# Kernel tuning notes

Measured on AMD Instinct MI355X. Metric: run time of the kernel, lower is better.

## Reference

```python
import jax, jax.numpy as jnp
import numpy as np

N = 50000
E = 640000
F_IN = 96
H1 = 128
H2 = 128
NUM_CLASSES = 256
NGRAM = 3
D1 = 32
L2_EPS = 1e-12


def _prop(xt, src, dst, ew):
    # weighted scatter-add aggregation: out[dst] += ew * xt[src]
    return jax.ops.segment_sum(ew[:, None] * xt[src], dst, num_segments=N)


def _digcn_layer(x, W_mi, W_mo, W_sk, b_mi, b_mo, b_si, b_so, C_in, C_out,
                 ei_in, ew_in, ei_out, ew_out):
    x_sk = x @ W_sk  # skip transform shared by in/out branches
    ic = (_prop(x @ W_mi, ei_in[0], ei_in[1], ew_in) + b_mi
          + _prop(x_sk, ei_in[0], ei_in[1], ew_in) + b_si)
    oc = (_prop(x @ W_mo, ei_out[0], ei_out[1], ew_out) + b_mo
          + _prop(x_sk, ei_out[0], ei_out[1], ew_out) + b_so)
    return C_in * ic + C_out * oc  # C_* are [N,1] vector coefficients


def setup_inputs() -> dict:
    key = jax.random.key(0)
    ks = jax.random.split(key, 32)
    s = 0.05
    d = {
        'x': jax.random.normal(ks[0], (N, F_IN), dtype=jnp.float32),
        'edge_index_in': jax.random.randint(ks[1], (2, E), 0, N, dtype=jnp.int32),
        'edge_weight_in': jax.random.uniform(ks[2], (E,), dtype=jnp.float32),
        'edge_index_out': jax.random.randint(ks[3], (2, E), 0, N, dtype=jnp.int32),
        'edge_weight_out': jax.random.uniform(ks[4], (E,), dtype=jnp.float32),
        'pe_table': jax.random.normal(ks[5], (NGRAM, D1), dtype=jnp.float32) * s,
    }
    dims = [(F_IN, H1), (H1, H1), (H1, H2)]
    ki = 6
    for li, (di, do) in enumerate(dims, start=1):
        d[f'W{li}_main_in'] = jax.random.normal(ks[ki], (di, do), dtype=jnp.float32) * s; ki += 1
        d[f'W{li}_main_out'] = jax.random.normal(ks[ki], (di, do), dtype=jnp.float32) * s; ki += 1
        d[f'W{li}_skip'] = jax.random.normal(ks[ki], (di, do), dtype=jnp.float32) * s; ki += 1
        d[f'b{li}_main_in'] = jax.random.normal(ks[ki], (do,), dtype=jnp.float32) * s; ki += 1
        d[f'b{li}_main_out'] = jax.random.normal(ks[ki], (do,), dtype=jnp.float32) * s; ki += 1
        d[f'b{li}_skip_in'] = jax.random.normal(ks[ki], (do,), dtype=jnp.float32) * s; ki += 1
        d[f'b{li}_skip_out'] = jax.random.normal(ks[ki], (do,), dtype=jnp.float32) * s; ki += 1
        d[f'C{li}_in'] = 1.0 + jax.random.normal(ks[ki], (N, 1), dtype=jnp.float32) * 0.02; ki += 1
        d[f'C{li}_out'] = 1.0 + jax.random.normal(ks[ki], (N, 1), dtype=jnp.float32) * 0.02; ki += 1
    k2 = jax.random.split(ks[ki], 4)
    d['res1_W'] = jax.random.normal(k2[0], (F_IN, H1), dtype=jnp.float32) * s
    d['res1_b'] = jax.random.normal(k2[1], (H1,), dtype=jnp.float32) * s
    d['dec_W'] = jax.random.normal(k2[2], (H2, NUM_CLASSES), dtype=jnp.float32) * s
    d['dec_b'] = jax.random.normal(k2[3], (NUM_CLASSES,), dtype=jnp.float32) * s
    return d


def reference(x, edge_index_in, edge_weight_in, edge_index_out, edge_weight_out, pe_table,
              W1_main_in, W1_main_out, W1_skip, b1_main_in, b1_main_out, b1_skip_in, b1_skip_out, C1_in, C1_out,
              W2_main_in, W2_main_out, W2_skip, b2_main_in, b2_main_out, b2_skip_in, b2_skip_out, C2_in, C2_out,
              W3_main_in, W3_main_out, W3_skip, b3_main_in, b3_main_out, b3_skip_in, b3_skip_out, C3_in, C3_out,
              res1_W, res1_b, dec_W, dec_b):
    # learnable positional encoding: x viewed as [N, ngram, d1] + pe[pos]
    x = (x.reshape(-1, NGRAM, D1) + pe_table[None]).reshape(-1, NGRAM * D1)

    h1 = _digcn_layer(x, W1_main_in, W1_main_out, W1_skip, b1_main_in, b1_main_out,
                      b1_skip_in, b1_skip_out, C1_in, C1_out,
                      edge_index_in, edge_weight_in, edge_index_out, edge_weight_out)
    h1 = jax.nn.relu(h1 + (x @ res1_W + res1_b))  # residual_proj_1 (96 -> 128)

    h2 = _digcn_layer(h1, W2_main_in, W2_main_out, W2_skip, b2_main_in, b2_main_out,
                      b2_skip_in, b2_skip_out, C2_in, C2_out,
                      edge_index_in, edge_weight_in, edge_index_out, edge_weight_out)
    h2 = jax.nn.relu(h2 + h1)  # identity residual (128 == 128)

    h3 = _digcn_layer(h2, W3_main_in, W3_main_out, W3_skip, b3_main_in, b3_main_out,
                      b3_skip_in, b3_skip_out, C3_in, C3_out,
                      edge_index_in, edge_weight_in, edge_index_out, edge_weight_out)
    h3 = h3 + h2  # residual_proj_3 is Identity (hidden1 == hidden2)

    norm = jnp.maximum(jnp.linalg.norm(h3, axis=1, keepdims=True), L2_EPS)
    emb = h3 / norm  # F.normalize, eps=1e-12
    logits = emb @ dec_W + dec_b
    return jax.nn.log_softmax(logits, axis=-1), emb
```

## Files before the change

kernel.cpp:

```cpp
#include <hip/hip_runtime.h>
#include <hip/hip_bf16.h>

typedef unsigned short ushort_t;
typedef __attribute__((ext_vector_type(8))) short bf16x8;
typedef __attribute__((ext_vector_type(4))) float f32x4;

__device__ __forceinline__ float bf2f(ushort_t u) {
    union { unsigned int i; float f; } v; v.i = ((unsigned int)u) << 16; return v.f;
}
__device__ __forceinline__ ushort_t f2bf(float f) {
    unsigned int u = __float_as_uint(f);
    unsigned int r = u + 0x7FFFu + ((u >> 16) & 1u);
    return (ushort_t)(r >> 16);
}
__device__ __forceinline__ float ldf(const void* p, size_t i, int isf) {
    return isf ? ((const float*)p)[i] : bf2f(((const ushort_t*)p)[i]);
}

__global__ void init_k(int* __restrict__ cntI, int* __restrict__ cntO, int n2,
                       const void* __restrict__ x, int* __restrict__ flag) {
    int i = blockIdx.x * 256 + threadIdx.x;
    if (i < n2) { cntI[i] = 0; cntO[i] = 0; }
    if (blockIdx.x == 0) {
        int t = threadIdx.x;
        const float* xf = (const float*)x;
        int bad = 0;
        for (int k = t; k < 2048; k += 256) {
            unsigned int u = __float_as_uint(xf[k]);
            unsigned int e = (u >> 23) & 0xFFu;
            if (e >= 0xC0u) bad = 1;
        }
        __shared__ int s_bad;
        if (t == 0) s_bad = 0;
        __syncthreads();
        if (bad) atomicOr(&s_bad, 1);
        __syncthreads();
        if (t == 0) flag[0] = s_bad ? 0 : 1;
    }
}

__global__ void count_both_k(const int* __restrict__ eiI, const int* __restrict__ eiO,
                             int* __restrict__ cntI, int* __restrict__ cntO,
                             int E, int egrid) {
    int set = blockIdx.x >= egrid ? 1 : 0;
    int e = (blockIdx.x - set * egrid) * 256 + threadIdx.x;
    if (e >= E) return;
    const int* ei = set ? eiO : eiI;
    int* cnt = set ? cntO : cntI;
    atomicAdd(&cnt[ei[E + e]], 1);
}

__global__ __launch_bounds__(256) void scan1_k(const int* __restrict__ cntA, const int* __restrict__ cntB,
                                               int* __restrict__ offA, int* __restrict__ offB,
                                               int* __restrict__ sums, int n, int nChunks) {
    int set = blockIdx.y;
    const int* cnt = set ? cntB : cntA;
    int* off = set ? offB : offA;
    __shared__ int s[256];
    int t = threadIdx.x;
    int idx = blockIdx.x * 1024 + t * 4;
    int v[4];
#pragma unroll
    for (int i = 0; i < 4; ++i) v[i] = (idx + i < n) ? cnt[idx + i] : 0;
    int tsum = v[0] + v[1] + v[2] + v[3];
    s[t] = tsum;
    __syncthreads();
    for (int d = 1; d < 256; d <<= 1) {
        int x = (t >= d) ? s[t - d] : 0;
        __syncthreads();
        s[t] += x;
        __syncthreads();
    }
    int run = s[t] - tsum;
    if (t == 255) sums[set * nChunks + blockIdx.x] = s[255];
#pragma unroll
    for (int i = 0; i < 4; ++i) { if (idx + i < n) off[idx + i] = run; run += v[i]; }
}

__global__ __launch_bounds__(256) void scan2_k(int* __restrict__ sums, int nChunks) {
    __shared__ int s[256];
    int t = threadIdx.x;
    for (int set = 0; set < 2; ++set) {
        int v = (t < nChunks) ? sums[set * nChunks + t] : 0;
        s[t] = v;
        __syncthreads();
        for (int d = 1; d < 256; d <<= 1) {
            int x = (t >= d) ? s[t - d] : 0;
            __syncthreads();
            s[t] += x;
            __syncthreads();
        }
        if (t < nChunks) sums[set * nChunks + t] = s[t] - v;
        __syncthreads();
    }
}

__global__ __launch_bounds__(256) void scan3_k(int* __restrict__ offA, int* __restrict__ offB,
                                               const int* __restrict__ sums, int n, int nChunks, int E) {
    int set = blockIdx.y;
    int* off = set ? offB : offA;
    int base = sums[set * nChunks + blockIdx.x];
    int idx = blockIdx.x * 1024 + threadIdx.x * 4;
#pragma unroll
    for (int i = 0; i < 4; ++i) { if (idx + i < n) off[idx + i] += base; }
    if (blockIdx.x == 0 && threadIdx.x == 0) off[n] = E;
}

__global__ void fill_both_k(const int* __restrict__ eiI, const void* __restrict__ ewI,
                            const int* __restrict__ eiO, const void* __restrict__ ewO,
                            const int* __restrict__ offI, const int* __restrict__ offO,
                            int* __restrict__ curI, int* __restrict__ curO,
                            uint2* __restrict__ prI, uint2* __restrict__ prO,
                            int E, int egrid, const int* __restrict__ flagp) {
    int isf = *flagp;
    int set = blockIdx.x >= egrid ? 1 : 0;
    int e = (blockIdx.x - set * egrid) * 256 + threadIdx.x;
    if (e >= E) return;
    const int* ei = set ? eiO : eiI;
    const void* ew = set ? ewO : ewI;
    const int* off = set ? offO : offI;
    int* cur = set ? curO : curI;
    uint2* pr = set ? prO : prI;
    int d = ei[E + e];
    int p = off[d] + atomicAdd(&cur[d], 1);
    pr[p] = make_uint2((unsigned)ei[e], __float_as_uint(ldf(ew, e, isf)));
}

struct PrepJob { const void* A; const void* B; ushort_t* dst; int K; int colOff; int cshift; int n; int blkBase; };
struct PrepJobsT { PrepJob j[8]; };
__global__ __launch_bounds__(256) void prep_all_k(PrepJobsT jobs, const int* __restrict__ flagp) {
    int isf = *flagp;
    int b = blockIdx.x;
    int ji = 0;
#pragma unroll
    for (int t = 1; t < 8; ++t) if (b >= jobs.j[t].blkBase) ji = t;
    PrepJob jb = jobs.j[ji];
    int i = (b - jb.blkBase) * 256 + threadIdx.x;
    if (i >= jb.n) return;
    int cmask = (1 << jb.cshift) - 1;
    int k = i >> jb.cshift, c = i & cmask;
    int Cw = cmask + 1;
    float v = ldf(jb.A, (size_t)k * Cw + c, isf);
    if (jb.B) v += ldf(jb.B, (size_t)k * Cw + c, isf);
    jb.dst[(size_t)(jb.colOff + c) * jb.K + k] = f2bf(v);
}

struct BiasJob { const void* a; const void* b; float* dst; int n; };
struct BiasJobs { BiasJob j[8]; };
__global__ void prep_bias_k(BiasJobs jobs, const int* __restrict__ flagp) {
    int isf = *flagp;
    BiasJob jb = jobs.j[blockIdx.x];
    int t = threadIdx.x;
    if (t < jb.n) {
        float v = ldf(jb.a, t, isf);
        if (jb.b) v += ldf(jb.b, t, isf);
        jb.dst[t] = v;
    }
}

template<int K, int DOUT>
__global__ __launch_bounds__(256) void gemm_mfma_k(
    const ushort_t* __restrict__ A, const ushort_t* __restrict__ Wt,
    ushort_t* __restrict__ Y, int M) {
    constexpr int NT = DOUT / 16;
    int tid = threadIdx.x;
    int wave = tid >> 6, lane = tid & 63;
    int q = lane >> 4, l15 = lane & 15;
    int arow = blockIdx.x * 64 + wave * 16 + l15;
    int rowc = arow < M ? arow : M - 1;
    f32x4 acc[NT];
#pragma unroll
    for (int t = 0; t < NT; ++t) acc[t] = (f32x4){0.f, 0.f, 0.f, 0.f};
#pragma unroll
    for (int kc = 0; kc < K; kc += 32) {
        bf16x8 a = *(const bf16x8*)(A + (size_t)rowc * K + kc + q * 8);
#pragma unroll
        for (int t = 0; t < NT; ++t) {
            bf16x8 b = *(const bf16x8*)(Wt + (size_t)(t * 16 + l15) * K + kc + q * 8);
            acc[t] = __builtin_amdgcn_mfma_f32_16x16x32_bf16(a, b, acc[t], 0, 0, 0);
        }
    }
    int outRowBase = blockIdx.x * 64 + wave * 16 + q * 4;
#pragma unroll
    for (int t = 0; t < NT; ++t) {
        int col = t * 16 + l15;
#pragma unroll
        for (int i = 0; i < 4; ++i) {
            int r = outRowBase + i;
            if (r < M) Y[(size_t)r * DOUT + col] = f2bf(acc[t][i]);
        }
    }
}

__global__ __launch_bounds__(256) void gemm_mfma_x_k(
    const void* __restrict__ X, const ushort_t* __restrict__ Wt,
    ushort_t* __restrict__ Y, int M, const void* __restrict__ pe,
    const int* __restrict__ flagp) {
    constexpr int K = 96, DOUT = 384, NT = DOUT / 16;
    __shared__ float pes[96];
    int isf = *flagp;
    int tid = threadIdx.x;
    if (tid < 96) pes[tid] = ldf(pe, tid, isf);
    __syncthreads();
    int wave = tid >> 6, lane = tid & 63;
    int q = lane >> 4, l15 = lane & 15;
    int arow = blockIdx.x * 64 + wave * 16 + l15;
    int rowc = arow < M ? arow : M - 1;
    f32x4 acc[NT];
#pragma unroll
    for (int t = 0; t < NT; ++t) acc[t] = (f32x4){0.f, 0.f, 0.f, 0.f};
#pragma unroll
    for (int kc = 0; kc < K; kc += 32) {
        float va[8];
        size_t base = (size_t)rowc * K + kc + q * 8;
        if (isf) {
            float4 u0 = *(const float4*)((const float*)X + base);
            float4 u1 = *(const float4*)((const float*)X + base + 4);
            va[0] = u0.x; va[1] = u0.y; va[2] = u0.z; va[3] = u0.w;
            va[4] = u1.x; va[5] = u1.y; va[6] = u1.z; va[7] = u1.w;
        } else {
            const ushort_t* xp = (const ushort_t*)X + base;
#pragma unroll
            for (int i = 0; i < 8; ++i) va[i] = bf2f(xp[i]);
        }
        bf16x8 a;
        short* ap = (short*)&a;
#pragma unroll
        for (int i = 0; i < 8; ++i) ap[i] = (short)f2bf(va[i] + pes[kc + q * 8 + i]);
#pragma unroll
        for (int t = 0; t < NT; ++t) {
            bf16x8 b = *(const bf16x8*)(Wt + (size_t)(t * 16 + l15) * K + kc + q * 8);
            acc[t] = __builtin_amdgcn_mfma_f32_16x16x32_bf16(a, b, acc[t], 0, 0, 0);
        }
    }
    int outRowBase = blockIdx.x * 64 + wave * 16 + q * 4;
#pragma unroll
    for (int t = 0; t < NT; ++t) {
        int col = t * 16 + l15;
#pragma unroll
        for (int i = 0; i < 4; ++i) {
            int r = outRowBase + i;
            if (r < M) Y[(size_t)r * DOUT + col] = f2bf(acc[t][i]);
        }
    }
}

__device__ __forceinline__ void accum8(float* acc, uint4 v, float w) {
    unsigned u[4] = {v.x, v.y, v.z, v.w};
#pragma unroll
    for (int i = 0; i < 4; ++i) {
        acc[2 * i]     = fmaf(w, __uint_as_float(u[i] << 16), acc[2 * i]);
        acc[2 * i + 1] = fmaf(w, __uint_as_float(u[i] & 0xFFFF0000u), acc[2 * i + 1]);
    }
}

__global__ __launch_bounds__(256) void prop_combine_k(
    const ushort_t* __restrict__ Y, int ldY,
    const int* __restrict__ offI, const uint2* __restrict__ prI,
    const int* __restrict__ offO, const uint2* __restrict__ prO,
    const void* __restrict__ Cin, const void* __restrict__ Cout,
    const float* __restrict__ bin, const float* __restrict__ bout,
    const ushort_t* __restrict__ res, int ldR, int colR, const float* __restrict__ res_b,
    ushort_t* __restrict__ H, int M, int relu, const int* __restrict__ flagp) {
    int isf = *flagp;
    int node = blockIdx.x * 4 + (threadIdx.x >> 6);
    int lane = threadIdx.x & 63;
    if (node >= M) return;
    int half = lane >> 5;
    int subq = (lane >> 4) & 1;
    int li   = lane & 15;
    int eI0 = offI[node], eI1 = offI[node + 1];
    int eO0 = offO[node], eO1 = offO[node + 1];
    int e0 = half ? eO0 : eI0;
    int e1 = half ? eO1 : eI1;
    const uint2* pairs = half ? prO : prI;
    const ushort_t* rowbase = Y + half * 128 + li * 8;
    int lenMax = max(eI1 - eI0, eO1 - eO0);
    float acc[8];
#pragma unroll
    for (int k = 0; k < 8; ++k) acc[k] = 0.f;
    for (int it = 0; it < lenMax; it += 4) {
        int eeA = e0 + it + subq;
        int eeB = eeA + 2;
        bool mA = eeA < e1, mB = eeB < e1;
        uint2 pa, pb;
        uint4 va, vb;
        if (mA) { pa = pairs[eeA]; va = *(const uint4*)(rowbase + (size_t)pa.x * ldY); }
        if (mB) { pb = pairs[eeB]; vb = *(const uint4*)(rowbase + (size_t)pb.x * ldY); }
        if (mA) accum8(acc, va, __uint_as_float(pa.y));
        if (mB) accum8(acc, vb, __uint_as_float(pb.y));
    }
    float other[8];
#pragma unroll
    for (int k = 0; k < 8; ++k) {
        acc[k] += __shfl_xor(acc[k], 16, 64);
        other[k] = __shfl_xor(acc[k], 32, 64);
    }
    int j = li * 8;
    float ci = ldf(Cin, node, isf), co = ldf(Cout, node, isf);
    uint4 rv = *(const uint4*)(res + (size_t)node * ldR + colR + j);
    float4 b0 = *(const float4*)(bin + j);
    float4 b1 = *(const float4*)(bin + j + 4);
    float4 c0 = *(const float4*)(bout + j);
    float4 c1 = *(const float4*)(bout + j + 4);
    float binv[8]  = {b0.x, b0.y, b0.z, b0.w, b1.x, b1.y, b1.z, b1.w};
    float boutv[8] = {c0.x, c0.y, c0.z, c0.w, c1.x, c1.y, c1.z, c1.w};
    float rbv[8] = {0.f, 0.f, 0.f, 0.f, 0.f, 0.f, 0.f, 0.f};
    if (res_b) {
        float4 r0 = *(const float4*)(res_b + j);
        float4 r1 = *(const float4*)(res_b + j + 4);
        rbv[0] = r0.x; rbv[1] = r0.y; rbv[2] = r0.z; rbv[3] = r0.w;
        rbv[4] = r1.x; rbv[5] = r1.y; rbv[6] = r1.z; rbv[7] = r1.w;
    }
    unsigned rw[4] = {rv.x, rv.y, rv.z, rv.w};
    float vo[8];
#pragma unroll
    for (int k = 0; k < 8; ++k) {
        float aiv = half ? other[k] : acc[k];
        float aov = half ? acc[k] : other[k];
        float r = (k & 1) ? __uint_as_float(rw[k >> 1] & 0xFFFF0000u)
                          : __uint_as_float(rw[k >> 1] << 16);
        float v = ci * (aiv + binv[k]) + co * (aov + boutv[k]) + r + rbv[k];
        if (relu) v = fmaxf(v, 0.f);
        vo[k] = v;
    }
    if ((lane >> 4) == 0) {
        uint4 outv;
        unsigned* op = (unsigned*)&outv;
#pragma unroll
        for (int k = 0; k < 4; ++k)
            op[k] = ((unsigned)f2bf(vo[2 * k + 1]) << 16) | (unsigned)f2bf(vo[2 * k]);
        *(uint4*)(H + (size_t)node * 128 + j) = outv;
    }
}

__global__ __launch_bounds__(256) void decoder_mfma_k(
    const ushort_t* __restrict__ h3, const ushort_t* __restrict__ Wdt,
    const float* __restrict__ biasDec, void* __restrict__ d_out, int M,
    const int* __restrict__ flagp) {
    __shared__ ushort_t embLds[64 * 136];
    __shared__ float sb[256];
    int isf = *flagp;
    int tid = threadIdx.x;
    sb[tid] = biasDec[tid];
    int rowBase = blockIdx.x * 64;
    {
        int r = tid >> 2;
        int c0 = (tid & 3) * 32;
        int grow = rowBase + r;
        uint4 u[4] = {};
        if (grow < M) {
            const uint4* p = (const uint4*)(h3 + (size_t)grow * 128 + c0);
            u[0] = p[0]; u[1] = p[1]; u[2] = p[2]; u[3] = p[3];
        }
        float v[32];
#pragma unroll
        for (int b = 0; b < 4; ++b) {
            unsigned w[4] = {u[b].x, u[b].y, u[b].z, u[b].w};
#pragma unroll
            for (int i = 0; i < 4; ++i) {
                v[b * 8 + 2 * i]     = bf2f((ushort_t)(w[i] & 0xffffu));
                v[b * 8 + 2 * i + 1] = bf2f((ushort_t)(w[i] >> 16));
            }
        }
        float ss = 0.f;
#pragma unroll
        for (int i = 0; i < 32; ++i) ss += v[i] * v[i];
        ss += __shfl_xor(ss, 1, 64);
        ss += __shfl_xor(ss, 2, 64);
        float inv = 1.0f / fmaxf(sqrtf(ss), 1e-12f);
#pragma unroll
        for (int i = 0; i < 32; ++i) v[i] *= inv;
        unsigned* lp = (unsigned*)&embLds[r * 136 + c0];
#pragma unroll
        for (int i = 0; i < 16; ++i)
            lp[i] = ((unsigned)f2bf(v[2 * i + 1]) << 16) | (unsigned)f2bf(v[2 * i]);
        if (grow < M) {
            if (isf) {
                float* op = (float*)d_out + (size_t)M * 256 + (size_t)grow * 128 + c0;
#pragma unroll
                for (int i = 0; i < 32; ++i) op[i] = v[i];
            } else {
                unsigned* op = (unsigned*)((ushort_t*)d_out + (size_t)M * 256 + (size_t)grow * 128 + c0);
#pragma unroll
                for (int i = 0; i < 16; ++i)
                    op[i] = ((unsigned)f2bf(v[2 * i + 1]) << 16) | (unsigned)f2bf(v[2 * i]);
            }
        }
    }
    __syncthreads();
    int wave = tid >> 6, lane = tid & 63, q = lane >> 4, l15 = lane & 15;
    f32x4 acc[16];
#pragma unroll
    for (int t = 0; t < 16; ++t) acc[t] = (f32x4){0.f, 0.f, 0.f, 0.f};
    int ldsRow = wave * 16 + l15;
#pragma unroll
    for (int kc = 0; kc < 128; kc += 32) {
        bf16x8 a = *(const bf16x8*)(&embLds[ldsRow * 136 + kc + q * 8]);
#pragma unroll
        for (int t = 0; t < 16; ++t) {
            bf16x8 b = *(const bf16x8*)(Wdt + (size_t)(t * 16 + l15) * 128 + kc + q * 8);
            acc[t] = __builtin_amdgcn_mfma_f32_16x16x32_bf16(a, b, acc[t], 0, 0, 0);
        }
    }
#pragma unroll
    for (int t = 0; t < 16; ++t) {
        float b = sb[t * 16 + l15];
        acc[t][0] += b; acc[t][1] += b; acc[t][2] += b; acc[t][3] += b;
    }
#pragma unroll
    for (int i = 0; i < 4; ++i) {
        int grow = rowBase + wave * 16 + q * 4 + i;
        float mx = acc[0][i];
#pragma unroll
        for (int t = 1; t < 16; ++t) mx = fmaxf(mx, acc[t][i]);
        mx = fmaxf(mx, __shfl_xor(mx, 1, 64));
        mx = fmaxf(mx, __shfl_xor(mx, 2, 64));
        mx = fmaxf(mx, __shfl_xor(mx, 4, 64));
        mx = fmaxf(mx, __shfl_xor(mx, 8, 64));
        float sm = 0.f;
#pragma unroll
        for (int t = 0; t < 16; ++t) sm += __expf(acc[t][i] - mx);
        sm += __shfl_xor(sm, 1, 64);
        sm += __shfl_xor(sm, 2, 64);
        sm += __shfl_xor(sm, 4, 64);
        sm += __shfl_xor(sm, 8, 64);
        float offv = mx + __logf(sm);
        if (grow < M) {
            if (isf) {
                float* op = (float*)d_out + (size_t)grow * 256 + l15;
#pragma unroll
                for (int t = 0; t < 16; ++t) op[t * 16] = acc[t][i] - offv;
            } else {
                ushort_t* op = (ushort_t*)d_out + (size_t)grow * 256 + l15;
#pragma unroll
                for (int t = 0; t < 16; ++t) op[t * 16] = f2bf(acc[t][i] - offv);
            }
        }
    }
}

extern "C" void kernel_launch(void* const* d_in, const int* in_sizes, int n_in,
                              void* d_out, int out_size, void* d_ws, size_t ws_size,
                              hipStream_t stream) {
    const int N = in_sizes[0] / 96;
    const int E = in_sizes[2];

    const void* x      = d_in[0];
    const int*  ei_in  = (const int*)d_in[1];
    const void* ew_in  = d_in[2];
    const int*  ei_out = (const int*)d_in[3];
    const void* ew_out = d_in[4];
    const void* pe     = d_in[5];

    const void *W_mi[3], *W_mo[3], *W_sk[3], *b_mi[3], *b_mo[3], *b_si[3], *b_so[3], *C_i[3], *C_o[3];
    for (int l = 0; l < 3; ++l) {
        int base = 6 + l * 9;
        W_mi[l] = d_in[base + 0];
        W_mo[l] = d_in[base + 1];
        W_sk[l] = d_in[base + 2];
        b_mi[l] = d_in[base + 3];
        b_mo[l] = d_in[base + 4];
        b_si[l] = d_in[base + 5];
        b_so[l] = d_in[base + 6];
        C_i[l]  = d_in[base + 7];
        C_o[l]  = d_in[base + 8];
    }
    const void* res1_W = d_in[33];
    const void* res1_b = d_in[34];
    const void* dec_W  = d_in[35];
    const void* dec_b  = d_in[36];

    char* ws = (char*)d_ws;
    size_t off = 0;
    auto alloc = [&](size_t bytes) -> void* {
        void* p = ws + off;
        off = (off + bytes + 255) & ~(size_t)255;
        return p;
    };
    const int nChunks = (N + 1023) / 1024;
    int*   flag    = (int*)alloc(4);
    int*   off_in  = (int*)alloc((size_t)(N + 1) * 4);
    int*   cnt_in  = (int*)alloc((size_t)2 * N * 4);
    int*   cur_in  = cnt_in + N;
    uint2* pr_in   = (uint2*)alloc((size_t)E * 8);
    int*   off_out = (int*)alloc((size_t)(N + 1) * 4);
    int*   cnt_out = (int*)alloc((size_t)2 * N * 4);
    int*   cur_out = cnt_out + N;
    uint2* pr_out  = (uint2*)alloc((size_t)E * 8);
    int*   sums    = (int*)alloc((size_t)2 * nChunks * 4);
    ushort_t* Wt1  = (ushort_t*)alloc((size_t)384 * 96 * 2);
    ushort_t* Wt2  = (ushort_t*)alloc((size_t)256 * 128 * 2);
    ushort_t* Wt3  = (ushort_t*)alloc((size_t)256 * 128 * 2);
    ushort_t* Wdt  = (ushort_t*)alloc((size_t)256 * 128 * 2);
    float* biasBlk = (float*)alloc((size_t)1152 * 4);
    float* bin1 = biasBlk, *bout1 = biasBlk + 128, *bin2 = biasBlk + 256, *bout2 = biasBlk + 384;
    float* bin3 = biasBlk + 512, *bout3 = biasBlk + 640, *res1b = biasBlk + 768, *decb = biasBlk + 896;
    ushort_t* Yb  = (ushort_t*)alloc((size_t)N * 384 * 2);
    ushort_t* H1  = (ushort_t*)alloc((size_t)N * 128 * 2);
    ushort_t* H2  = (ushort_t*)alloc((size_t)N * 128 * 2);
    ushort_t* H3  = H1;

    {
        int n2 = 2 * N;
        int g = (n2 + 255) / 256;
        init_k<<<g, 256, 0, stream>>>(cnt_in, cnt_out, n2, x, flag);
    }

    int egrid = (E + 255) / 256;
    count_both_k<<<2 * egrid, 256, 0, stream>>>(ei_in, ei_out, cnt_in, cnt_out, E, egrid);
    {
        dim3 g(nChunks, 2);
        scan1_k<<<g, 256, 0, stream>>>(cnt_in, cnt_out, off_in, off_out, sums, N, nChunks);
        scan2_k<<<1, 256, 0, stream>>>(sums, nChunks);
        scan3_k<<<g, 256, 0, stream>>>(off_in, off_out, sums, N, nChunks, E);
    }
    fill_both_k<<<2 * egrid, 256, 0, stream>>>(ei_in, ew_in, ei_out, ew_out,
        off_in, off_out, cur_in, cur_out, pr_in, pr_out, E, egrid, flag);

    {
        PrepJobsT pj;
        pj.j[0] = {W_mi[0], W_sk[0], Wt1, 96, 0,   7, 128 * 96, 0};
        pj.j[1] = {W_mo[0], W_sk[0], Wt1, 96, 128, 7, 128 * 96, 48};
        pj.j[2] = {res1_W, nullptr,  Wt1, 96, 256, 7, 128 * 96, 96};
        pj.j[3] = {W_mi[1], W_sk[1], Wt2, 128, 0,   7, 128 * 128, 144};
        pj.j[4] = {W_mo[1], W_sk[1], Wt2, 128, 128, 7, 128 * 128, 208};
        pj.j[5] = {W_mi[2], W_sk[2], Wt3, 128, 0,   7, 128 * 128, 272};
        pj.j[6] = {W_mo[2], W_sk[2], Wt3, 128, 128, 7, 128 * 128, 336};
        pj.j[7] = {dec_W, nullptr, Wdt, 128, 0, 8, 32768, 400};
        prep_all_k<<<528, 256, 0, stream>>>(pj, flag);
    }
    {
        BiasJobs jb;
        jb.j[0] = {b_mi[0], b_si[0], bin1, 128};
        jb.j[1] = {b_mo[0], b_so[0], bout1, 128};
        jb.j[2] = {b_mi[1], b_si[1], bin2, 128};
        jb.j[3] = {b_mo[1], b_so[1], bout2, 128};
        jb.j[4] = {b_mi[2], b_si[2], bin3, 128};
        jb.j[5] = {b_mo[2], b_so[2], bout3, 128};
        jb.j[6] = {res1_b, nullptr, res1b, 128};
        jb.j[7] = {dec_b, nullptr, decb, 256};
        prep_bias_k<<<8, 256, 0, stream>>>(jb, flag);
    }

    int gBlocks = (N + 63) / 64;
    int pgrid = (N + 3) / 4;

    gemm_mfma_x_k<<<gBlocks, 256, 0, stream>>>(x, Wt1, Yb, N, pe, flag);
    prop_combine_k<<<pgrid, 256, 0, stream>>>(Yb, 384,
        off_in, pr_in, off_out, pr_out,
        C_i[0], C_o[0], bin1, bout1, Yb, 384, 256, res1b, H1, N, 1, flag);
    gemm_mfma_k<128, 256><<<gBlocks, 256, 0, stream>>>(H1, Wt2, Yb, N);
    prop_combine_k<<<pgrid, 256, 0, stream>>>(Yb, 256,
        off_in, pr_in, off_out, pr_out,
        C_i[1], C_o[1], bin2, bout2, H1, 128, 0, (const float*)nullptr, H2, N, 1, flag);
    gemm_mfma_k<128, 256><<<gBlocks, 256, 0, stream>>>(H2, Wt3, Yb, N);
    prop_combine_k<<<pgrid, 256, 0, stream>>>(Yb, 256,
        off_in, pr_in, off_out, pr_out,
        C_i[2], C_o[2], bin3, bout3, H2, 128, 0, (const float*)nullptr, H3, N, 0, flag);
    decoder_mfma_k<<<gBlocks, 256, 0, stream>>>(H3, Wdt, decb, d_out, N, flag);
}
```

Baseline: 643.2 us.

## Build CSR via two-level bucketed binning with shared-memory histograms

Replaces per-node global atomic counting, the three-pass scan, and per-edge atomic scatter fill with a two-level counting sort. Edges are first binned into 64-node buckets using shared-memory histograms and one global atomic per bucket per block. A per-bucket kernel then sorts entries by local node in shared memory and writes the node offsets. This aims to cut global atomic contention and scattered writes during CSR construction. In exchange it adds a temporary buffer (aliased onto Yb), packs the local node id into the high bits of src (assumes src < 2^26), and relies on NB ≤ 1024 for the single-block scan.

```diff
diff --git a/kernel.cpp b/kernel.cpp
--- a/kernel.cpp
+++ b/kernel.cpp
@@ -17,10 +17,11 @@
     return isf ? ((const float*)p)[i] : bf2f(((const ushort_t*)p)[i]);
 }
 
-__global__ void init_k(int* __restrict__ cntI, int* __restrict__ cntO, int n2,
+__global__ void init_k(int* __restrict__ bcntI, int* __restrict__ bcntO,
+                       int* __restrict__ bcurI, int* __restrict__ bcurO, int NB,
                        const void* __restrict__ x, int* __restrict__ flag) {
     int i = blockIdx.x * 256 + threadIdx.x;
-    if (i < n2) { cntI[i] = 0; cntO[i] = 0; }
+    if (i < NB) { bcntI[i] = 0; bcntO[i] = 0; bcurI[i] = 0; bcurO[i] = 0; }
     if (blockIdx.x == 0) {
         int t = threadIdx.x;
         const float* xf = (const float*)x;
@@ -39,50 +40,44 @@
     }
 }
 
-__global__ void count_both_k(const int* __restrict__ eiI, const int* __restrict__ eiO,
-                             int* __restrict__ cntI, int* __restrict__ cntO,
-                             int E, int egrid) {
-    int set = blockIdx.x >= egrid ? 1 : 0;
-    int e = (blockIdx.x - set * egrid) * 256 + threadIdx.x;
-    if (e >= E) return;
+
+__global__ __launch_bounds__(256) void csr_count_k(
+    const int* __restrict__ eiI, const int* __restrict__ eiO,
+    int* __restrict__ bcntI, int* __restrict__ bcntO, int E, int nblk) {
+    int set = blockIdx.x >= nblk ? 1 : 0;
+    int blk = blockIdx.x - set * nblk;
     const int* ei = set ? eiO : eiI;
-    int* cnt = set ? cntO : cntI;
-    atomicAdd(&cnt[ei[E + e]], 1);
-}
-
-__global__ __launch_bounds__(256) void scan1_k(const int* __restrict__ cntA, const int* __restrict__ cntB,
-                                               int* __restrict__ offA, int* __restrict__ offB,
-                                               int* __restrict__ sums, int n, int nChunks) {
-    int set = blockIdx.y;
-    const int* cnt = set ? cntB : cntA;
-    int* off = set ? offB : offA;
-    __shared__ int s[256];
+    int* bcnt = set ? bcntO : bcntI;
+    __shared__ unsigned hist[1024];
     int t = threadIdx.x;
-    int idx = blockIdx.x * 1024 + t * 4;
-    int v[4];
-#pragma unroll
-    for (int i = 0; i < 4; ++i) v[i] = (idx + i < n) ? cnt[idx + i] : 0;
-    int tsum = v[0] + v[1] + v[2] + v[3];
-    s[t] = tsum;
-    __syncthreads();
-    for (int d = 1; d < 256; d <<= 1) {
-        int x = (t >= d) ? s[t - d] : 0;
-        __syncthreads();
-        s[t] += x;
-        __syncthreads();
-    }
-    int run = s[t] - tsum;
-    if (t == 255) sums[set * nChunks + blockIdx.x] = s[255];
-#pragma unroll
-    for (int i = 0; i < 4; ++i) { if (idx + i < n) off[idx + i] = run; run += v[i]; }
-}
-
-__global__ __launch_bounds__(256) void scan2_k(int* __restrict__ sums, int nChunks) {
+    for (int i = t; i < 1024; i += 256) hist[i] = 0;
+    __syncthreads();
+    int e0 = blk * 8192;
+    for (int i = t; i < 8192; i += 256) {
+        int e = e0 + i;
+        if (e < E) atomicAdd(&hist[((unsigned)ei[E + e]) >> 6], 1u);
+    }
+    __syncthreads();
+    for (int b = t; b < 1024; b += 256) {
+        unsigned c = hist[b];
+        if (c) atomicAdd(&bcnt[b], (int)c);
+    }
+}
+
+__global__ __launch_bounds__(256) void csr_scan_k(
+    const int* __restrict__ bcntI, const int* __restrict__ bcntO,
+    int* __restrict__ bstartI, int* __restrict__ bstartO, int NB, int E) {
     __shared__ int s[256];
     int t = threadIdx.x;
     for (int set = 0; set < 2; ++set) {
-        int v = (t < nChunks) ? sums[set * nChunks + t] : 0;
-        s[t] = v;
+        const int* bcnt = set ? bcntO : bcntI;
+        int* bstart = set ? bstartO : bstartI;
+        int idx = t * 4;
+        int v[4];
+#pragma unroll
+        for (int i = 0; i < 4; ++i) v[i] = (idx + i < NB) ? bcnt[idx + i] : 0;
+        int tsum = v[0] + v[1] + v[2] + v[3];
+        s[t] = tsum;
         __syncthreads();
         for (int d = 1; d < 256; d <<= 1) {
             int x = (t >= d) ? s[t - d] : 0;
@@ -90,40 +85,99 @@
             s[t] += x;
             __syncthreads();
         }
-        if (t < nChunks) sums[set * nChunks + t] = s[t] - v;
+        int run = s[t] - tsum;
+#pragma unroll
+        for (int i = 0; i < 4; ++i) { if (idx + i < NB) bstart[idx + i] = run; run += v[i]; }
+        if (t == 0) bstart[NB] = E;
         __syncthreads();
     }
 }
 
-__global__ __launch_bounds__(256) void scan3_k(int* __restrict__ offA, int* __restrict__ offB,
-                                               const int* __restrict__ sums, int n, int nChunks, int E) {
-    int set = blockIdx.y;
-    int* off = set ? offB : offA;
-    int base = sums[set * nChunks + blockIdx.x];
-    int idx = blockIdx.x * 1024 + threadIdx.x * 4;
-#pragma unroll
-    for (int i = 0; i < 4; ++i) { if (idx + i < n) off[idx + i] += base; }
-    if (blockIdx.x == 0 && threadIdx.x == 0) off[n] = E;
-}
-
-__global__ void fill_both_k(const int* __restrict__ eiI, const void* __restrict__ ewI,
-                            const int* __restrict__ eiO, const void* __restrict__ ewO,
-                            const int* __restrict__ offI, const int* __restrict__ offO,
-                            int* __restrict__ curI, int* __restrict__ curO,
-                            uint2* __restrict__ prI, uint2* __restrict__ prO,
-                            int E, int egrid, const int* __restrict__ flagp) {
+__global__ __launch_bounds__(256) void csr_bin_k(
+    const int* __restrict__ eiI, const void* __restrict__ ewI,
+    const int* __restrict__ eiO, const void* __restrict__ ewO,
+    const int* __restrict__ bstartI, const int* __restrict__ bstartO,
+    int* __restrict__ bcurI, int* __restrict__ bcurO,
+    uint2* __restrict__ tmpI, uint2* __restrict__ tmpO,
+    int E, int nblk, int NB, const int* __restrict__ flagp) {
     int isf = *flagp;
-    int set = blockIdx.x >= egrid ? 1 : 0;
-    int e = (blockIdx.x - set * egrid) * 256 + threadIdx.x;
-    if (e >= E) return;
+    int set = blockIdx.x >= nblk ? 1 : 0;
+    int blk = blockIdx.x - set * nblk;
     const int* ei = set ? eiO : eiI;
     const void* ew = set ? ewO : ewI;
-    const int* off = set ? offO : offI;
-    int* cur = set ? curO : curI;
+    const int* bstart = set ? bstartO : bstartI;
+    int* bcur = set ? bcurO : bcurI;
+    uint2* tmp = set ? tmpO : tmpI;
+    __shared__ unsigned hist[1024];
+    __shared__ unsigned hbase[1024];
+    int t = threadIdx.x;
+    int e0 = blk * 8192;
+    for (int i = t; i < 1024; i += 256) hist[i] = 0;
+    __syncthreads();
+    for (int i = t; i < 8192; i += 256) {
+        int e = e0 + i;
+        if (e < E) atomicAdd(&hist[((unsigned)ei[E + e]) >> 6], 1u);
+    }
+    __syncthreads();
+    for (int b = t; b < NB; b += 256) {
+        unsigned c = hist[b];
+        hbase[b] = c ? (unsigned)atomicAdd(&bcur[b], (int)c) : 0u;
+    }
+    __syncthreads();
+    for (int i = t; i < 1024; i += 256) hist[i] = 0;
+    __syncthreads();
+    for (int i = t; i < 8192; i += 256) {
+        int e = e0 + i;
+        if (e < E) {
+            unsigned d = (unsigned)ei[E + e];
+            unsigned b = d >> 6;
+            unsigned r = atomicAdd(&hist[b], 1u);
+            unsigned src = (unsigned)ei[e];
+            unsigned wb = __float_as_uint(ldf(ew, e, isf));
+            tmp[bstart[b] + hbase[b] + r] = make_uint2(src | ((d & 63u) << 26), wb);
+        }
+    }
+}
+
+__global__ __launch_bounds__(256) void csr_final_k(
+    const uint2* __restrict__ tmpI, const uint2* __restrict__ tmpO,
+    const int* __restrict__ bstartI, const int* __restrict__ bstartO,
+    uint2* __restrict__ prI, uint2* __restrict__ prO,
+    int* __restrict__ offI, int* __restrict__ offO,
+    int N, int E, int NB) {
+    int set = blockIdx.x >= NB ? 1 : 0;
+    int b = blockIdx.x - set * NB;
+    const uint2* tmp = set ? tmpO : tmpI;
+    const int* bstart = set ? bstartO : bstartI;
     uint2* pr = set ? prO : prI;
-    int d = ei[E + e];
-    int p = off[d] + atomicAdd(&cur[d], 1);
-    pr[p] = make_uint2((unsigned)ei[e], __float_as_uint(ldf(ew, e, isf)));
+    int* off = set ? offO : offI;
+    int s0 = bstart[b], s1 = bstart[b + 1];
+    int cnt = s1 - s0;
+    __shared__ unsigned ndc[64];
+    __shared__ unsigned pref[64];
+    __shared__ unsigned ncur[64];
+    int t = threadIdx.x;
+    if (t < 64) { ndc[t] = 0; ncur[t] = 0; }
+    __syncthreads();
+    for (int i = t; i < cnt; i += 256)
+        atomicAdd(&ndc[tmp[s0 + i].x >> 26], 1u);
+    __syncthreads();
+    if (t == 0) {
+        unsigned run = 0;
+        for (int i = 0; i < 64; ++i) { pref[i] = run; run += ndc[i]; }
+    }
+    __syncthreads();
+    if (t < 64) {
+        int node = b * 64 + t;
+        if (node < N) off[node] = s0 + (int)pref[t];
+    }
+    if (b == 0 && t == 0) off[N] = E;
+    for (int i = t; i < cnt; i += 256) {
+        uint2 en = tmp[s0 + i];
+        unsigned dl = en.x >> 26;
+        unsigned r = atomicAdd(&ncur[dl], 1u);
+        pr[s0 + (int)(pref[dl] + r)] = make_uint2(en.x & 0x03FFFFFFu, en.y);
+    }
 }
 
 struct PrepJob { const void* A; const void* B; ushort_t* dst; int K; int colOff; int cshift; int n; int blkBase; };
@@ -478,17 +532,18 @@
         off = (off + bytes + 255) & ~(size_t)255;
         return p;
     };
-    const int nChunks = (N + 1023) / 1024;
+    const int NB = (N + 63) / 64;
     int*   flag    = (int*)alloc(4);
     int*   off_in  = (int*)alloc((size_t)(N + 1) * 4);
-    int*   cnt_in  = (int*)alloc((size_t)2 * N * 4);
-    int*   cur_in  = cnt_in + N;
+    int*   off_out = (int*)alloc((size_t)(N + 1) * 4);
     uint2* pr_in   = (uint2*)alloc((size_t)E * 8);
-    int*   off_out = (int*)alloc((size_t)(N + 1) * 4);
-    int*   cnt_out = (int*)alloc((size_t)2 * N * 4);
-    int*   cur_out = cnt_out + N;
     uint2* pr_out  = (uint2*)alloc((size_t)E * 8);
-    int*   sums    = (int*)alloc((size_t)2 * nChunks * 4);
+    int*   bcntI   = (int*)alloc((size_t)NB * 4);
+    int*   bcntO   = (int*)alloc((size_t)NB * 4);
+    int*   bcurI   = (int*)alloc((size_t)NB * 4);
+    int*   bcurO   = (int*)alloc((size_t)NB * 4);
+    int*   bstartI = (int*)alloc((size_t)(NB + 1) * 4);
+    int*   bstartO = (int*)alloc((size_t)(NB + 1) * 4);
     ushort_t* Wt1  = (ushort_t*)alloc((size_t)384 * 96 * 2);
     ushort_t* Wt2  = (ushort_t*)alloc((size_t)256 * 128 * 2);
     ushort_t* Wt3  = (ushort_t*)alloc((size_t)256 * 128 * 2);
@@ -500,23 +555,22 @@
     ushort_t* H1  = (ushort_t*)alloc((size_t)N * 128 * 2);
     ushort_t* H2  = (ushort_t*)alloc((size_t)N * 128 * 2);
     ushort_t* H3  = H1;
+    uint2* tmpI = (uint2*)Yb;
+    uint2* tmpO = tmpI + E;
 
     {
-        int n2 = 2 * N;
-        int g = (n2 + 255) / 256;
-        init_k<<<g, 256, 0, stream>>>(cnt_in, cnt_out, n2, x, flag);
-    }
-
-    int egrid = (E + 255) / 256;
-    count_both_k<<<2 * egrid, 256, 0, stream>>>(ei_in, ei_out, cnt_in, cnt_out, E, egrid);
-    {
-        dim3 g(nChunks, 2);
-        scan1_k<<<g, 256, 0, stream>>>(cnt_in, cnt_out, off_in, off_out, sums, N, nChunks);
-        scan2_k<<<1, 256, 0, stream>>>(sums, nChunks);
-        scan3_k<<<g, 256, 0, stream>>>(off_in, off_out, sums, N, nChunks, E);
-    }
-    fill_both_k<<<2 * egrid, 256, 0, stream>>>(ei_in, ew_in, ei_out, ew_out,
-        off_in, off_out, cur_in, cur_out, pr_in, pr_out, E, egrid, flag);
+        int g = (NB + 255) / 256;
+        init_k<<<g, 256, 0, stream>>>(bcntI, bcntO, bcurI, bcurO, NB, x, flag);
+    }
+
+    const int EB = 8192;
+    int nblk = (E + EB - 1) / EB;
+    csr_count_k<<<2 * nblk, 256, 0, stream>>>(ei_in, ei_out, bcntI, bcntO, E, nblk);
+    csr_scan_k<<<1, 256, 0, stream>>>(bcntI, bcntO, bstartI, bstartO, NB, E);
+    csr_bin_k<<<2 * nblk, 256, 0, stream>>>(ei_in, ew_in, ei_out, ew_out,
+        bstartI, bstartO, bcurI, bcurO, tmpI, tmpO, E, nblk, NB, flag);
+    csr_final_k<<<2 * NB, 256, 0, stream>>>(tmpI, tmpO, bstartI, bstartO,
+        pr_in, pr_out, off_in, off_out, N, E, NB);
 
     {
         PrepJobsT pj;
```

Measured after the change: 559.2 us. 13.1% less time.
